# Performance work log

Hardware: AMD Instinct MI355X
Metric: run time of the kernel (lower is better)

Reference implementation:

```python
import jax, jax.numpy as jnp
import numpy as np

D_EMBED = 1024
N_HEAD = 16
LEN_TRIM = 1024
LN_EPS = 1e-5


def setup_inputs() -> dict:
    key = jax.random.key(0)
    ks = jax.random.split(key, 8)
    B = 2
    h_q = jax.random.normal(ks[0], (B, LEN_TRIM, D_EMBED), jnp.float32)
    h_kv1 = jax.random.normal(ks[1], (B, LEN_TRIM, D_EMBED), jnp.float32)
    h_kv2 = jax.random.normal(ks[2], (B, 2 * LEN_TRIM, D_EMBED), jnp.float32)
    mask = jax.random.uniform(ks[3], (B, LEN_TRIM, 1), jnp.float32)
    in_proj_w = jax.random.normal(ks[4], (3 * D_EMBED, D_EMBED), jnp.float32) * 0.02
    in_proj_b = jnp.zeros((3 * D_EMBED,), jnp.float32)
    out_w = jax.random.normal(ks[5], (D_EMBED, D_EMBED), jnp.float32) * 0.02
    out_b = jnp.zeros((D_EMBED,), jnp.float32)
    ln_g = jnp.ones((D_EMBED,), jnp.float32)
    ln_b = jnp.zeros((D_EMBED,), jnp.float32)
    return dict(h_q=h_q, h_kv1=h_kv1, h_kv2=h_kv2, mask=mask,
                in_proj_w=in_proj_w, in_proj_b=in_proj_b,
                out_w=out_w, out_b=out_b, ln_g=ln_g, ln_b=ln_b)


def _layernorm(x, g, b):
    mu = jnp.mean(x, axis=-1, keepdims=True)
    var = jnp.mean(jnp.square(x - mu), axis=-1, keepdims=True)
    return (x - mu) * jax.lax.rsqrt(var + LN_EPS) * g + b


def reference(h_q, h_kv1, h_kv2, mask, in_proj_w, in_proj_b, out_w, out_b, ln_g, ln_b):
    B, L, D = h_q.shape
    H = N_HEAD
    dh = D // H
    h_kv = jnp.concatenate((h_kv1, h_kv2), axis=1)  # (B, 3L, D)
    S = h_kv.shape[1]
    Wq, Wk, Wv = jnp.split(in_proj_w, 3, axis=0)
    bq, bk, bv = jnp.split(in_proj_b, 3, axis=0)
    q = (h_q @ Wq.T + bq).reshape(B, L, H, dh).transpose(0, 2, 1, 3)   # (B,H,L,dh)
    k = (h_kv @ Wk.T + bk).reshape(B, S, H, dh).transpose(0, 2, 1, 3)  # (B,H,S,dh)
    v = (h_kv @ Wv.T + bv).reshape(B, S, H, dh).transpose(0, 2, 1, 3)
    scores = jnp.einsum('bhld,bhsd->bhls', q, k) / jnp.sqrt(jnp.float32(dh))
    block = jnp.triu(jnp.ones((L, L), bool), k=1)
    mask_causal = jnp.concatenate((block, block, block), axis=-1)  # (L, S)
    scores = jnp.where(mask_causal, -jnp.inf, scores)
    attn = jax.nn.softmax(scores, axis=-1)
    ctx = jnp.einsum('bhls,bhsd->bhld', attn, v).transpose(0, 2, 1, 3).reshape(B, L, D)
    attn_out = ctx @ out_w.T + out_b
    return _layernorm(h_q + attn_out, ln_g, ln_b) * mask
```

## Files before the change

kernel.cpp:

```cpp
#include <hip/hip_runtime.h>
#include <stdint.h>

typedef unsigned short u16;
typedef unsigned int u32;
typedef __bf16 bf16x8 __attribute__((ext_vector_type(8)));
typedef float floatx4 __attribute__((ext_vector_type(4)));
typedef u16 u16x8 __attribute__((ext_vector_type(8)));
typedef u16 u16x4 __attribute__((ext_vector_type(4)));

__device__ __forceinline__ u16 f2bf(float f) {
    __bf16 h = (__bf16)f;
    return __builtin_bit_cast(u16, h);
}

__device__ __forceinline__ void gll16(const u16* g, u16* l) {
    typedef __attribute__((address_space(1))) u32 gu32;
    typedef __attribute__((address_space(3))) u32 lu32;
    __builtin_amdgcn_global_load_lds((gu32*)g, (lu32*)l, 16, 0, 0);
}

__global__ __launch_bounds__(256) void cvt_all(const float* __restrict__ hq,
                                               const float* __restrict__ kv1,
                                               const float* __restrict__ kv2,
                                               const float* __restrict__ win,
                                               u16* __restrict__ a_q,
                                               u16* __restrict__ a_kv,
                                               u16* __restrict__ wb) {
    const int NQ = 262144, NKV = 786432, NW = 393216;
    int i = blockIdx.x * 256 + threadIdx.x;
    const int stride = gridDim.x * 256;
    for (; i < NQ + NKV + NW; i += stride) {
        const float* src; u16* dst;
        if (i < NQ) {
            src = hq + (long long)i * 8; dst = a_q + (long long)i * 8;
        } else if (i < NQ + NKV) {
            int c = i - NQ;
            int row = c >> 7;
            int col = (c & 127) * 8;
            int b = row >= 3072, r = row - b * 3072;
            src = (r < 1024) ? kv1 + ((long long)(b * 1024 + r)) * 1024 + col
                             : kv2 + ((long long)(b * 2048 + (r - 1024))) * 1024 + col;
            dst = a_kv + (long long)row * 1024 + col;
        } else {
            int c = i - (NQ + NKV);
            src = win + (long long)c * 8; dst = wb + (long long)c * 8;
        }
        floatx4 x = *(const floatx4*)src;
        floatx4 y = *(const floatx4*)(src + 4);
        u16x8 o;
        #pragma unroll
        for (int j = 0; j < 4; j++) { o[j] = f2bf(x[j]); o[4 + j] = f2bf(y[j]); }
        *(u16x8*)dst = o;
    }
}

__global__ __launch_bounds__(256) void cvt_bf16(const float* __restrict__ in,
                                                u16* __restrict__ out, int n8) {
    int i = blockIdx.x * 256 + threadIdx.x;
    const int stride = gridDim.x * 256;
    for (; i < n8; i += stride) {
        floatx4 a = *(const floatx4*)(in + (long long)i * 8);
        floatx4 b = *(const floatx4*)(in + (long long)i * 8 + 4);
        u16x8 o;
        #pragma unroll
        for (int j = 0; j < 4; j++) { o[j] = f2bf(a[j]); o[4 + j] = f2bf(b[j]); }
        *(u16x8*)(out + (long long)i * 8) = o;
    }
}

__global__ __launch_bounds__(256) void gemm_proj(const u16* __restrict__ aq,
                                                 const u16* __restrict__ akv,
                                                 const u16* __restrict__ wb,
                                                 const float* __restrict__ bias,
                                                 u16* __restrict__ Qo,
                                                 u16* __restrict__ Ko,
                                                 u16* __restrict__ VTg) {
    __shared__ u16 lds[2][2][8192];
    const int tid = threadIdx.x;
    const int wave = tid >> 6, lane = tid & 63;
    const int lane16 = lane & 15, quad = lane >> 4;
    const int bid = blockIdx.x;
    const int g = (bid & 7) * 112 + (bid >> 3);
    const bool qblk = g < 128;
    int my, nx;
    if (qblk) { my = g >> 3; nx = g & 7; }
    else { int gg = g - 128; my = gg >> 4; nx = gg & 15; }
    const int rowBase = my * 128;
    const int colBase = nx * 128;
    const int wrow = (qblk ? 0 : 1024) + colBase;
    const int wm = (wave >> 1) * 64, wn = (wave & 1) * 64;

    floatx4 acc[4][4];
    #pragma unroll
    for (int am = 0; am < 4; am++)
        #pragma unroll
        for (int bn = 0; bn < 4; bn++) acc[am][bn] = floatx4{0.f, 0.f, 0.f, 0.f};

    const int srow8 = tid >> 3;
    const int scol = ((tid & 7) ^ (srow8 & 7)) * 8;
    const u16* aS = (qblk ? aq : akv) + (long long)(rowBase + srow8) * 1024 + scol;
    const u16* bS = wb + (long long)(wrow + srow8) * 1024 + scol;
    u16* lbase = &lds[0][0][0];
    const int ldst = wave * 512;

    const int cko0 = ((quad ^ (lane16 & 7)) * 8);
    const int cko1 = (((4 + quad) ^ (lane16 & 7)) * 8);

    {
        u16* dA = lbase; u16* dB = lbase + 8192;
        #pragma unroll
        for (int j = 0; j < 4; j++) {
            gll16(aS + j * 32768, dA + j * 2048 + ldst);
            gll16(bS + j * 32768, dB + j * 2048 + ldst);
        }
    }
    __syncthreads();

    int buf = 0;
    for (int t = 0; t < 16; t++) {
        if (t < 15) {
            const int k0 = (t + 1) * 64;
            u16* dA = lbase + (buf ^ 1) * 16384;
            u16* dB = dA + 8192;
            #pragma unroll
            for (int j = 0; j < 4; j++) {
                gll16(aS + j * 32768 + k0, dA + j * 2048 + ldst);
                gll16(bS + j * 32768 + k0, dB + j * 2048 + ldst);
            }
        }
        const u16* Ab = lbase + buf * 16384;
        const u16* Bb = Ab + 8192;
        u16x8 a0[4], a1[4], b0[4], b1[4];
        #pragma unroll
        for (int i = 0; i < 4; i++) {
            a0[i] = *(const u16x8*)&Ab[(wm + i * 16 + lane16) * 64 + cko0];
            a1[i] = *(const u16x8*)&Ab[(wm + i * 16 + lane16) * 64 + cko1];
            b0[i] = *(const u16x8*)&Bb[(wn + i * 16 + lane16) * 64 + cko0];
            b1[i] = *(const u16x8*)&Bb[(wn + i * 16 + lane16) * 64 + cko1];
        }
        #pragma unroll
        for (int am = 0; am < 4; am++)
            #pragma unroll
            for (int bn = 0; bn < 4; bn++)
                acc[am][bn] = __builtin_amdgcn_mfma_f32_16x16x32_bf16(
                    __builtin_bit_cast(bf16x8, a0[am]),
                    __builtin_bit_cast(bf16x8, b0[bn]), acc[am][bn], 0, 0, 0);
        #pragma unroll
        for (int am = 0; am < 4; am++)
            #pragma unroll
            for (int bn = 0; bn < 4; bn++)
                acc[am][bn] = __builtin_amdgcn_mfma_f32_16x16x32_bf16(
                    __builtin_bit_cast(bf16x8, a1[am]),
                    __builtin_bit_cast(bf16x8, b1[bn]), acc[am][bn], 0, 0, 0);
        __syncthreads();
        buf ^= 1;
    }

    const float* bcol = bias + (qblk ? 0 : 1024) + colBase;
    if (qblk || nx < 8) {
        u16* Cb = qblk ? Qo : Ko;
        #pragma unroll
        for (int am = 0; am < 4; am++)
            #pragma unroll
            for (int bn = 0; bn < 4; bn++)
                #pragma unroll
                for (int r = 0; r < 4; r++) {
                    int row = rowBase + wm + am * 16 + quad * 4 + r;
                    int col = wn + bn * 16 + lane16;
                    float v = acc[am][bn][r] + bcol[col];
                    Cb[(long long)row * 1024 + colBase + col] = f2bf(v);
                }
    } else {
        const int b_ = rowBase >= 3072;
        const int keyBase = rowBase - b_ * 3072 + wm;
        #pragma unroll
        for (int am = 0; am < 4; am++)
            #pragma unroll
            for (int bn = 0; bn < 4; bn++) {
                int col = wn + bn * 16 + lane16;
                int d = colBase - 1024 + col;
                int key0 = keyBase + am * 16 + quad * 4;
                u16x4 pk;
                #pragma unroll
                for (int r = 0; r < 4; r++) pk[r] = f2bf(acc[am][bn][r] + bcol[col]);
                *(u16x4*)&VTg[((long long)(b_ * 1024 + d)) * 3072 + key0] = pk;
            }
    }
}

__global__ __launch_bounds__(256) void gemm_out(const u16* __restrict__ ctx,
                                                const u16* __restrict__ wob,
                                                const float* __restrict__ bias,
                                                float* __restrict__ ao0,
                                                float* __restrict__ ao1) {
    __shared__ u16 lds[2][2][8192];
    const int tid = threadIdx.x;
    const int wave = tid >> 6, lane = tid & 63;
    const int lane16 = lane & 15, quad = lane >> 4;
    const int bid = blockIdx.x;
    const int g = (bid & 7) * 32 + (bid >> 3);
    const int my = g >> 4;
    const int nx = (g & 15) >> 1;
    const int kh = g & 1;
    const int rowBase = my * 128, colBase = nx * 128, kbase = kh * 512;
    const int wm = (wave >> 1) * 64, wn = (wave & 1) * 64;

    floatx4 acc[4][4];
    #pragma unroll
    for (int am = 0; am < 4; am++)
        #pragma unroll
        for (int bn = 0; bn < 4; bn++) acc[am][bn] = floatx4{0.f, 0.f, 0.f, 0.f};

    const int srow8 = tid >> 3;
    const int scol = ((tid & 7) ^ (srow8 & 7)) * 8;
    const u16* aS = ctx + (long long)(rowBase + srow8) * 1024 + kbase + scol;
    const u16* bS = wob + (long long)(colBase + srow8) * 1024 + kbase + scol;
    u16* lbase = &lds[0][0][0];
    const int ldst = wave * 512;
    const int cko0 = ((quad ^ (lane16 & 7)) * 8);
    const int cko1 = (((4 + quad) ^ (lane16 & 7)) * 8);

    {
        u16* dA = lbase; u16* dB = lbase + 8192;
        #pragma unroll
        for (int j = 0; j < 4; j++) {
            gll16(aS + j * 32768, dA + j * 2048 + ldst);
            gll16(bS + j * 32768, dB + j * 2048 + ldst);
        }
    }
    __syncthreads();

    int buf = 0;
    for (int t = 0; t < 8; t++) {
        if (t < 7) {
            const int k0 = (t + 1) * 64;
            u16* dA = lbase + (buf ^ 1) * 16384;
            u16* dB = dA + 8192;
            #pragma unroll
            for (int j = 0; j < 4; j++) {
                gll16(aS + j * 32768 + k0, dA + j * 2048 + ldst);
                gll16(bS + j * 32768 + k0, dB + j * 2048 + ldst);
            }
        }
        const u16* Ab = lbase + buf * 16384;
        const u16* Bb = Ab + 8192;
        u16x8 a0[4], a1[4], b0[4], b1[4];
        #pragma unroll
        for (int i = 0; i < 4; i++) {
            a0[i] = *(const u16x8*)&Ab[(wm + i * 16 + lane16) * 64 + cko0];
            a1[i] = *(const u16x8*)&Ab[(wm + i * 16 + lane16) * 64 + cko1];
            b0[i] = *(const u16x8*)&Bb[(wn + i * 16 + lane16) * 64 + cko0];
            b1[i] = *(const u16x8*)&Bb[(wn + i * 16 + lane16) * 64 + cko1];
        }
        #pragma unroll
        for (int am = 0; am < 4; am++)
            #pragma unroll
            for (int bn = 0; bn < 4; bn++)
                acc[am][bn] = __builtin_amdgcn_mfma_f32_16x16x32_bf16(
                    __builtin_bit_cast(bf16x8, a0[am]),
                    __builtin_bit_cast(bf16x8, b0[bn]), acc[am][bn], 0, 0, 0);
        #pragma unroll
        for (int am = 0; am < 4; am++)
            #pragma unroll
            for (int bn = 0; bn < 4; bn++)
                acc[am][bn] = __builtin_amdgcn_mfma_f32_16x16x32_bf16(
                    __builtin_bit_cast(bf16x8, a1[am]),
                    __builtin_bit_cast(bf16x8, b1[bn]), acc[am][bn], 0, 0, 0);
        __syncthreads();
        buf ^= 1;
    }

    float* Co = kh ? ao1 : ao0;
    #pragma unroll
    for (int am = 0; am < 4; am++)
        #pragma unroll
        for (int bn = 0; bn < 4; bn++)
            #pragma unroll
            for (int r = 0; r < 4; r++) {
                int row = rowBase + wm + am * 16 + quad * 4 + r;
                int col = colBase + wn + bn * 16 + lane16;
                float v = acc[am][bn][r] + (kh == 0 ? bias[col] : 0.f);
                Co[(long long)row * 1024 + col] = v;
            }
}

__global__ __launch_bounds__(256) void attn_seg(const u16* __restrict__ Q,
                                                const u16* __restrict__ Kb,
                                                const u16* __restrict__ VTg,
                                                float* __restrict__ pO_lo,
                                                float* __restrict__ pO_hi,
                                                float* __restrict__ pml) {
    __shared__ u16 Kt[2][4096];
    __shared__ u16 Vt[2][4096];
    __shared__ u16 Ps[4][1280];
    const int tid = threadIdx.x;
    const int wave = tid >> 6, lane = tid & 63;
    const int lane16 = lane & 15, quad = lane >> 4;
    const int bid = blockIdx.x;
    const int idx_ = (bid & 7) * 192 + (bid >> 3);
    const int qhat = idx_ & 15;
    const int h   = (idx_ >> 4) & 15;
    const int b   = (idx_ >> 8) & 1;
    const int seg = idx_ >> 9;
    const int qt = b ? (15 - qhat) : qhat;
    const int l0 = qt * 64;
    const int wq = wave * 16;
    const float scale = 0.125f;

    bf16x8 qf[2];
    {
        const u16* qrow = Q + ((long long)(b * 1024 + l0 + wq + lane16)) * 1024 + h * 64;
        qf[0] = __builtin_bit_cast(bf16x8, *(const u16x8*)(qrow + quad * 8));
        qf[1] = __builtin_bit_cast(bf16x8, *(const u16x8*)(qrow + 32 + quad * 8));
    }

    const int srow = tid >> 3;
    const int csw8 = ((tid & 7) ^ (srow & 7)) * 8;
    const long long bh = ((long long)b * 3072) * 1024 + h * 64;
    const u16* kS = Kb + bh + ((long long)(seg * 1024)) * 1024
                    + (long long)srow * 1024 + csw8;
    const u16* vS = VTg + ((long long)(b * 1024 + h * 64 + srow)) * 3072
                    + seg * 1024 + csw8;
    const int ldst = wave * 512;

    {
        #pragma unroll
        for (int j = 0; j < 2; j++) {
            gll16(kS + j * 32768, &Kt[0][j * 2048 + ldst]);
            gll16(vS + (long long)j * 32 * 3072, &Vt[0][j * 2048 + ldst]);
        }
    }
    __syncthreads();

    const int slot0 = ((quad ^ (lane16 & 7)) * 8);
    const int slot1 = (((4 + quad) ^ (lane16 & 7)) * 8);

    float m_i = -1e30f, l_i = 0.f;
    floatx4 o_acc[4];
    #pragma unroll
    for (int mi = 0; mi < 4; mi++) o_acc[mi] = floatx4{0.f, 0.f, 0.f, 0.f};

    for (int t = 0; t <= qt; t++) {
        const int cur = t & 1;
        const bool haveNext = t < qt;

        if (haveNext) {
            const long long ko = (long long)(t + 1) * 65536;
            const long long vo = (long long)(t + 1) * 64;
            #pragma unroll
            for (int j = 0; j < 2; j++) {
                gll16(kS + ko + j * 32768, &Kt[cur ^ 1][j * 2048 + ldst]);
                gll16(vS + vo + (long long)j * 32 * 3072, &Vt[cur ^ 1][j * 2048 + ldst]);
            }
        }

        floatx4 sacc[4];
        #pragma unroll
        for (int mi = 0; mi < 4; mi++) sacc[mi] = floatx4{0.f, 0.f, 0.f, 0.f};
        #pragma unroll
        for (int mi = 0; mi < 4; mi++) {
            u16x8 kf = *(const u16x8*)&Kt[cur][(mi * 16 + lane16) * 64 + slot0];
            sacc[mi] = __builtin_amdgcn_mfma_f32_16x16x32_bf16(
                __builtin_bit_cast(bf16x8, kf), qf[0], sacc[mi], 0, 0, 0);
        }
        #pragma unroll
        for (int mi = 0; mi < 4; mi++) {
            u16x8 kf = *(const u16x8*)&Kt[cur][(mi * 16 + lane16) * 64 + slot1];
            sacc[mi] = __builtin_amdgcn_mfma_f32_16x16x32_bf16(
                __builtin_bit_cast(bf16x8, kf), qf[1], sacc[mi], 0, 0, 0);
        }

        const bool diag = (t == qt);
        const int qloc = wq + lane16;
        float tmax = -1e30f;
        #pragma unroll
        for (int mi = 0; mi < 4; mi++)
            #pragma unroll
            for (int r = 0; r < 4; r++) {
                float s = sacc[mi][r] * scale;
                if (diag && (mi * 16 + quad * 4 + r) > qloc) s = -1e30f;
                sacc[mi][r] = s;
                tmax = fmaxf(tmax, s);
            }
        tmax = fmaxf(tmax, __shfl_xor(tmax, 16));
        tmax = fmaxf(tmax, __shfl_xor(tmax, 32));
        float m_new = fmaxf(m_i, tmax);
        float alpha = __expf(m_i - m_new);
        float psum = 0.f;
        #pragma unroll
        for (int mi = 0; mi < 4; mi++) {
            u16x4 pk;
            #pragma unroll
            for (int r = 0; r < 4; r++) {
                float p = __expf(sacc[mi][r] - m_new);
                psum += p;
                pk[r] = f2bf(p);
            }
            *(u16x4*)&Ps[wave][lane16 * 80 + mi * 16 + quad * 4] = pk;
        }
        psum += __shfl_xor(psum, 16);
        psum += __shfl_xor(psum, 32);
        m_i = m_new;
        l_i = l_i * alpha + psum;
        #pragma unroll
        for (int mi = 0; mi < 4; mi++)
            #pragma unroll
            for (int r = 0; r < 4; r++) o_acc[mi][r] *= alpha;

        __builtin_amdgcn_wave_barrier();

        #pragma unroll
        for (int c = 0; c < 2; c++) {
            bf16x8 pf = __builtin_bit_cast(bf16x8,
                *(const u16x8*)&Ps[wave][lane16 * 80 + c * 32 + quad * 8]);
            const int slot = c ? slot1 : slot0;
            #pragma unroll
            for (int mi = 0; mi < 4; mi++) {
                bf16x8 vf = __builtin_bit_cast(bf16x8,
                    *(const u16x8*)&Vt[cur][(mi * 16 + lane16) * 64 + slot]);
                o_acc[mi] = __builtin_amdgcn_mfma_f32_16x16x32_bf16(vf, pf, o_acc[mi], 0, 0, 0);
            }
        }

        if (haveNext) __syncthreads();
    }

    const int p = ((b * 16 + h) * 16 + qt) * 3 + seg;
    float* op = (p < 512) ? (pO_lo + (long long)p * 4096)
                          : (pO_hi + (long long)(p - 512) * 4096);
    if (quad == 0) {
        pml[(long long)p * 128 + (wq + lane16) * 2]     = m_i;
        pml[(long long)p * 128 + (wq + lane16) * 2 + 1] = l_i;
    }
    float* orow = op + (long long)(wq + lane16) * 64;
    #pragma unroll
    for (int mi = 0; mi < 4; mi++)
        *(floatx4*)(orow + mi * 16 + quad * 4) = o_acc[mi];
}

__global__ __launch_bounds__(256) void attn_combine(const float* __restrict__ pO_lo,
                                                    const float* __restrict__ pO_hi,
                                                    const float* __restrict__ pml,
                                                    u16* __restrict__ Ctx) {
    const int g = blockIdx.x;
    const int qt = g & 15;
    const int h  = (g >> 4) & 15;
    const int b  = g >> 8;
    const int t  = threadIdx.x;
    const int q  = t >> 2;
    const int d0 = (t & 3) * 16;
    const int p0 = g * 3;

    float m[3], l[3];
    #pragma unroll
    for (int s = 0; s < 3; s++) {
        m[s] = pml[(long long)(p0 + s) * 128 + q * 2];
        l[s] = pml[(long long)(p0 + s) * 128 + q * 2 + 1];
    }
    float M = fmaxf(m[0], fmaxf(m[1], m[2]));
    float w[3];
    #pragma unroll
    for (int s = 0; s < 3; s++) w[s] = __expf(m[s] - M);
    float L = w[0] * l[0] + w[1] * l[1] + w[2] * l[2];
    float invL = 1.0f / L;

    const float* O[3];
    #pragma unroll
    for (int s = 0; s < 3; s++) {
        int pp = p0 + s;
        O[s] = ((pp < 512) ? (pO_lo + (long long)pp * 4096)
                           : (pO_hi + (long long)(pp - 512) * 4096))
               + (long long)q * 64 + d0;
    }

    long long crow = ((long long)(b * 1024 + qt * 64 + q)) * 1024 + h * 64 + d0;
    #pragma unroll
    for (int i = 0; i < 16; i += 4) {
        floatx4 a  = *(const floatx4*)(O[0] + i);
        floatx4 bb = *(const floatx4*)(O[1] + i);
        floatx4 cc = *(const floatx4*)(O[2] + i);
        #pragma unroll
        for (int j = 0; j < 4; j++)
            Ctx[crow + i + j] = f2bf((w[0] * a[j] + w[1] * bb[j] + w[2] * cc[j]) * invL);
    }
}

__global__ __launch_bounds__(256) void ln_kernel(const float* __restrict__ AO0,
                                                 const float* __restrict__ AO1,
                                                 const float* __restrict__ HQ,
                                                 const float* __restrict__ g,
                                                 const float* __restrict__ bb,
                                                 const float* __restrict__ mask,
                                                 float* __restrict__ Out) {
    const int row = blockIdx.x;
    const int t = threadIdx.x;
    const int base = row * 1024 + t * 4;
    floatx4 a0 = *(const floatx4*)&AO0[base];
    floatx4 a1 = *(const floatx4*)&AO1[base];
    floatx4 hq = *(const floatx4*)&HQ[base];
    float x[4];
    #pragma unroll
    for (int i = 0; i < 4; i++) x[i] = a0[i] + a1[i] + hq[i];
    float s = x[0] + x[1] + x[2] + x[3];
    float ss = x[0]*x[0] + x[1]*x[1] + x[2]*x[2] + x[3]*x[3];
    #pragma unroll
    for (int off = 32; off >= 1; off >>= 1) { s += __shfl_xor(s, off); ss += __shfl_xor(ss, off); }
    __shared__ float smem[8];
    int wave = t >> 6, lane = t & 63;
    if (lane == 0) { smem[wave] = s; smem[4 + wave] = ss; }
    __syncthreads();
    s  = smem[0] + smem[1] + smem[2] + smem[3];
    ss = smem[4] + smem[5] + smem[6] + smem[7];
    float mu  = s * (1.f / 1024.f);
    float var = ss * (1.f / 1024.f) - mu * mu;
    float rs  = rsqrtf(var + 1e-5f);
    float mv  = mask[row];
    floatx4 g4 = *(const floatx4*)&g[t * 4];
    floatx4 b4 = *(const floatx4*)&bb[t * 4];
    floatx4 y4;
    #pragma unroll
    for (int i = 0; i < 4; i++) y4[i] = ((x[i] - mu) * rs * g4[i] + b4[i]) * mv;
    *(floatx4*)&Out[base] = y4;
}

extern "C" void kernel_launch(void* const* d_in, const int* in_sizes, int n_in,
                              void* d_out, int out_size, void* d_ws, size_t ws_size,
                              hipStream_t stream) {
    (void)in_sizes; (void)n_in; (void)out_size; (void)ws_size;
    const float* h_q   = (const float*)d_in[0];
    const float* h_kv1 = (const float*)d_in[1];
    const float* h_kv2 = (const float*)d_in[2];
    const float* maskp = (const float*)d_in[3];
    const float* win   = (const float*)d_in[4];
    const float* binp  = (const float*)d_in[5];
    const float* wout  = (const float*)d_in[6];
    const float* bout  = (const float*)d_in[7];
    const float* ln_g  = (const float*)d_in[8];
    const float* ln_b  = (const float*)d_in[9];
    float* outp = (float*)d_out;

    char* ws = (char*)d_ws;
    const size_t MB = 1024 * 1024;
    u16*   q_b   = (u16*)(ws);
    u16*   k_b   = (u16*)(ws + 4 * MB);
    u16*   vT    = (u16*)(ws + 16 * MB);
    u16*   ctx_b = q_b;
    u16*   a_q   = (u16*)(ws + 28 * MB);
    u16*   a_kv  = (u16*)(ws + 32 * MB);
    u16*   wb    = (u16*)d_out;
    float* pO_lo = (float*)d_out;
    float* pO_hi = (float*)(ws + 28 * MB);
    u16*   wob   = (u16*)(ws + 28 * MB);
    float* pml   = (float*)(ws + 44 * MB);
    float* ao0   = (float*)(ws + 4 * MB);
    float* ao1   = (float*)(ws + 12 * MB);

    cvt_all<<<2048, 256, 0, stream>>>(h_q, h_kv1, h_kv2, win, a_q, a_kv, wb);
    gemm_proj<<<896, 256, 0, stream>>>(a_q, a_kv, wb, binp, q_b, k_b, vT);
    attn_seg<<<1536, 256, 0, stream>>>(q_b, k_b, vT, pO_lo, pO_hi, pml);
    attn_combine<<<512, 256, 0, stream>>>(pO_lo, pO_hi, pml, ctx_b);
    cvt_bf16<<<512, 256, 0, stream>>>(wout, wob, 131072);
    gemm_out<<<256, 256, 0, stream>>>(ctx_b, wob, bout, ao0, ao1);
    ln_kernel<<<2048, 256, 0, stream>>>(ao0, ao1, h_q, ln_g, ln_b, maskp, outp);
}
```

Before: 225.8 us.

## Streamline attention softmax with exp2, lazy rescale, split diagonal tile, priorities

The attention inner loop becomes a macro instantiated separately for off-diagonal and diagonal tiles, which removes the per-iteration mask branch. Scores are pre-scaled by log2(e)/8 so exp2 replaces expf. The running-max rescale of the output accumulators is skipped while the new max stays within 8 of the current one, and the row-sum reduction across lanes moves out of the loop to the end. It also adds s_setprio around the MFMA blocks and pads the P buffer stride against LDS bank conflicts; the combine kernel now uses exp2 to match the base-2 max values.

```diff
diff --git a/kernel.cpp b/kernel.cpp
--- a/kernel.cpp
+++ b/kernel.cpp
@@ -284,6 +284,86 @@
             }
 }
 
+#define ATTN_TILE(DIAG_, HAVENEXT_)                                           \
+{                                                                             \
+    const int cur = t & 1;                                                    \
+    if (HAVENEXT_) {                                                          \
+        const long long ko = (long long)(t + 1) * 65536;                      \
+        const long long vo = (long long)(t + 1) * 64;                         \
+        _Pragma("unroll")                                                     \
+        for (int j = 0; j < 2; j++) {                                         \
+            gll16(kS + ko + j * 32768, &Kt[cur ^ 1][j * 2048 + ldst]);        \
+            gll16(vS + vo + (long long)j * 32 * 3072, &Vt[cur ^ 1][j * 2048 + ldst]); \
+        }                                                                     \
+    }                                                                         \
+    floatx4 sacc[4];                                                          \
+    _Pragma("unroll")                                                         \
+    for (int mi = 0; mi < 4; mi++) sacc[mi] = floatx4{0.f, 0.f, 0.f, 0.f};    \
+    __builtin_amdgcn_s_setprio(1);                                            \
+    _Pragma("unroll")                                                         \
+    for (int mi = 0; mi < 4; mi++) {                                          \
+        u16x8 kf = *(const u16x8*)&Kt[cur][(mi * 16 + lane16) * 64 + slot0];  \
+        sacc[mi] = __builtin_amdgcn_mfma_f32_16x16x32_bf16(                   \
+            __builtin_bit_cast(bf16x8, kf), qf[0], sacc[mi], 0, 0, 0);        \
+    }                                                                         \
+    _Pragma("unroll")                                                         \
+    for (int mi = 0; mi < 4; mi++) {                                          \
+        u16x8 kf = *(const u16x8*)&Kt[cur][(mi * 16 + lane16) * 64 + slot1];  \
+        sacc[mi] = __builtin_amdgcn_mfma_f32_16x16x32_bf16(                   \
+            __builtin_bit_cast(bf16x8, kf), qf[1], sacc[mi], 0, 0, 0);        \
+    }                                                                         \
+    __builtin_amdgcn_s_setprio(0);                                            \
+    float tmax = -1e30f;                                                      \
+    _Pragma("unroll")                                                         \
+    for (int mi = 0; mi < 4; mi++)                                            \
+        _Pragma("unroll")                                                     \
+        for (int r = 0; r < 4; r++) {                                         \
+            float s = sacc[mi][r] * C2;                                       \
+            if (DIAG_ && (mi * 16 + quad * 4 + r) > qloc) s = -1e30f;         \
+            sacc[mi][r] = s;                                                  \
+            tmax = fmaxf(tmax, s);                                            \
+        }                                                                     \
+    tmax = fmaxf(tmax, __shfl_xor(tmax, 16));                                 \
+    tmax = fmaxf(tmax, __shfl_xor(tmax, 32));                                 \
+    if (!__all(tmax <= m_i + 8.0f)) {           \
+        float m_new = fmaxf(m_i, tmax);                                       \
+        float alpha = exp2f(m_i - m_new);                                     \
+        _Pragma("unroll")                                                     \
+        for (int mi = 0; mi < 4; mi++)                                        \
+            _Pragma("unroll")                                                 \
+            for (int r = 0; r < 4; r++) o_acc[mi][r] *= alpha;                \
+        l_lane *= alpha;                                                      \
+        m_i = m_new;                                                          \
+    }                                                                         \
+    _Pragma("unroll")                                                         \
+    for (int mi = 0; mi < 4; mi++) {                                          \
+        u16x4 pk;                                                             \
+        _Pragma("unroll")                                                     \
+        for (int r = 0; r < 4; r++) {                                         \
+            float p = exp2f(sacc[mi][r] - m_i);                               \
+            l_lane += p;                                                      \
+            pk[r] = f2bf(p);                                                  \
+        }                                                                     \
+        *(u16x4*)&Ps[wave][lane16 * 84 + mi * 16 + quad * 4] = pk;            \
+    }                                                                         \
+    __builtin_amdgcn_wave_barrier();                                          \
+    __builtin_amdgcn_s_setprio(1);                                            \
+    _Pragma("unroll")                                                         \
+    for (int c = 0; c < 2; c++) {                                             \
+        bf16x8 pf = __builtin_bit_cast(bf16x8,                                \
+            *(const u16x8*)&Ps[wave][lane16 * 84 + c * 32 + quad * 8]);       \
+        const int slot = c ? slot1 : slot0;                                   \
+        _Pragma("unroll")                                                     \
+        for (int mi = 0; mi < 4; mi++) {                                      \
+            bf16x8 vf = __builtin_bit_cast(bf16x8,                            \
+                *(const u16x8*)&Vt[cur][(mi * 16 + lane16) * 64 + slot]);     \
+            o_acc[mi] = __builtin_amdgcn_mfma_f32_16x16x32_bf16(vf, pf, o_acc[mi], 0, 0, 0); \
+        }                                                                     \
+    }                                                                         \
+    __builtin_amdgcn_s_setprio(0);                                            \
+    if (HAVENEXT_) __syncthreads();                                           \
+}
+
 __global__ __launch_bounds__(256) void attn_seg(const u16* __restrict__ Q,
                                                 const u16* __restrict__ Kb,
                                                 const u16* __restrict__ VTg,
@@ -292,7 +372,7 @@
                                                 float* __restrict__ pml) {
     __shared__ u16 Kt[2][4096];
     __shared__ u16 Vt[2][4096];
-    __shared__ u16 Ps[4][1280];
+    __shared__ u16 Ps[4][1344];
     const int tid = threadIdx.x;
     const int wave = tid >> 6, lane = tid & 63;
     const int lane16 = lane & 15, quad = lane >> 4;
@@ -305,7 +385,8 @@
     const int qt = b ? (15 - qhat) : qhat;
     const int l0 = qt * 64;
     const int wq = wave * 16;
-    const float scale = 0.125f;
+    const float C2 = 0.1803368801f;
+    const int qloc = wq + lane16;
 
     bf16x8 qf[2];
     {
@@ -335,95 +416,17 @@
     const int slot0 = ((quad ^ (lane16 & 7)) * 8);
     const int slot1 = (((4 + quad) ^ (lane16 & 7)) * 8);
 
-    float m_i = -1e30f, l_i = 0.f;
+    float m_i = -1e30f, l_lane = 0.f;
     floatx4 o_acc[4];
     #pragma unroll
     for (int mi = 0; mi < 4; mi++) o_acc[mi] = floatx4{0.f, 0.f, 0.f, 0.f};
 
-    for (int t = 0; t <= qt; t++) {
-        const int cur = t & 1;
-        const bool haveNext = t < qt;
-
-        if (haveNext) {
-            const long long ko = (long long)(t + 1) * 65536;
-            const long long vo = (long long)(t + 1) * 64;
-            #pragma unroll
-            for (int j = 0; j < 2; j++) {
-                gll16(kS + ko + j * 32768, &Kt[cur ^ 1][j * 2048 + ldst]);
-                gll16(vS + vo + (long long)j * 32 * 3072, &Vt[cur ^ 1][j * 2048 + ldst]);
-            }
-        }
-
-        floatx4 sacc[4];
-        #pragma unroll
-        for (int mi = 0; mi < 4; mi++) sacc[mi] = floatx4{0.f, 0.f, 0.f, 0.f};
-        #pragma unroll
-        for (int mi = 0; mi < 4; mi++) {
-            u16x8 kf = *(const u16x8*)&Kt[cur][(mi * 16 + lane16) * 64 + slot0];
-            sacc[mi] = __builtin_amdgcn_mfma_f32_16x16x32_bf16(
-                __builtin_bit_cast(bf16x8, kf), qf[0], sacc[mi], 0, 0, 0);
-        }
-        #pragma unroll
-        for (int mi = 0; mi < 4; mi++) {
-            u16x8 kf = *(const u16x8*)&Kt[cur][(mi * 16 + lane16) * 64 + slot1];
-            sacc[mi] = __builtin_amdgcn_mfma_f32_16x16x32_bf16(
-                __builtin_bit_cast(bf16x8, kf), qf[1], sacc[mi], 0, 0, 0);
-        }
-
-        const bool diag = (t == qt);
-        const int qloc = wq + lane16;
-        float tmax = -1e30f;
-        #pragma unroll
-        for (int mi = 0; mi < 4; mi++)
-            #pragma unroll
-            for (int r = 0; r < 4; r++) {
-                float s = sacc[mi][r] * scale;
-                if (diag && (mi * 16 + quad * 4 + r) > qloc) s = -1e30f;
-                sacc[mi][r] = s;
-                tmax = fmaxf(tmax, s);
-            }
-        tmax = fmaxf(tmax, __shfl_xor(tmax, 16));
-        tmax = fmaxf(tmax, __shfl_xor(tmax, 32));
-        float m_new = fmaxf(m_i, tmax);
-        float alpha = __expf(m_i - m_new);
-        float psum = 0.f;
-        #pragma unroll
-        for (int mi = 0; mi < 4; mi++) {
-            u16x4 pk;
-            #pragma unroll
-            for (int r = 0; r < 4; r++) {
-                float p = __expf(sacc[mi][r] - m_new);
-                psum += p;
-                pk[r] = f2bf(p);
-            }
-            *(u16x4*)&Ps[wave][lane16 * 80 + mi * 16 + quad * 4] = pk;
-        }
-        psum += __shfl_xor(psum, 16);
-        psum += __shfl_xor(psum, 32);
-        m_i = m_new;
-        l_i = l_i * alpha + psum;
-        #pragma unroll
-        for (int mi = 0; mi < 4; mi++)
-            #pragma unroll
-            for (int r = 0; r < 4; r++) o_acc[mi][r] *= alpha;
-
-        __builtin_amdgcn_wave_barrier();
-
-        #pragma unroll
-        for (int c = 0; c < 2; c++) {
-            bf16x8 pf = __builtin_bit_cast(bf16x8,
-                *(const u16x8*)&Ps[wave][lane16 * 80 + c * 32 + quad * 8]);
-            const int slot = c ? slot1 : slot0;
-            #pragma unroll
-            for (int mi = 0; mi < 4; mi++) {
-                bf16x8 vf = __builtin_bit_cast(bf16x8,
-                    *(const u16x8*)&Vt[cur][(mi * 16 + lane16) * 64 + slot]);
-                o_acc[mi] = __builtin_amdgcn_mfma_f32_16x16x32_bf16(vf, pf, o_acc[mi], 0, 0, 0);
-            }
-        }
-
-        if (haveNext) __syncthreads();
-    }
+    for (int t = 0; t < qt; t++) ATTN_TILE(false, true)
+    { int t = qt; ATTN_TILE(true, false) }
+
+    float l_i = l_lane;
+    l_i += __shfl_xor(l_i, 16);
+    l_i += __shfl_xor(l_i, 32);
 
     const int p = ((b * 16 + h) * 16 + qt) * 3 + seg;
     float* op = (p < 512) ? (pO_lo + (long long)p * 4096)
@@ -460,7 +463,7 @@
     float M = fmaxf(m[0], fmaxf(m[1], m[2]));
     float w[3];
     #pragma unroll
-    for (int s = 0; s < 3; s++) w[s] = __expf(m[s] - M);
+    for (int s = 0; s < 3; s++) w[s] = exp2f(m[s] - M);
     float L = w[0] * l[0] + w[1] * l[1] + w[2] * l[2];
     float invL = 1.0f / L;
 
```

After: 225.9 us. No clear change (+0.0%).
